# Optimization experiments

Hardware: AMD Instinct MI355X
Metric: run time of the kernel (lower is better)

## Reference

```python
import jax, jax.numpy as jnp
import numpy as np

B, T, H, DH = 4, 2048, 16, 64   # batch, block_size, num_head, chunk_size (per-head dim)
NE = H * DH                      # n_embed = 1024
EPS = 1e-5                       # torch GroupNorm default eps


def _decay_mask(T):
    # D[h, n, m] = gamma_h**(n-m) for n>=m else 0 (RetNet decay matrix)
    gamma = 1.0 - 2.0 ** (-5.0 - jnp.arange(H, dtype=jnp.float32))  # [H]
    idx = jnp.arange(T)
    diff = idx[:, None] - idx[None, :]                # [T, T]
    mask = diff >= 0
    expo = jnp.where(mask, diff, 0).astype(jnp.float32)
    D = (gamma[:, None, None] ** expo[None]) * mask[None].astype(jnp.float32)
    return gamma, D


def setup_inputs() -> dict:
    key = jax.random.key(0)
    ks = jax.random.split(key, 5)
    x = jax.random.normal(ks[0], (B, T, NE), jnp.float32)
    past_kv = jax.random.normal(ks[1], (H, DH, DH), jnp.float32)
    Wq = jax.random.normal(ks[2], (NE, NE), jnp.float32) * 0.02
    Wk = jax.random.normal(ks[3], (NE, NE), jnp.float32) * 0.02
    Wv = jax.random.normal(ks[4], (NE, NE), jnp.float32) * 0.02
    gn_w = jnp.ones((H,), jnp.float32)
    gn_b = jnp.zeros((H,), jnp.float32)
    return {"x": x, "past_kv": past_kv, "Wq": Wq, "Wk": Wk, "Wv": Wv,
            "gn_w": gn_w, "gn_b": gn_b}


def reference(x, past_kv, Wq, Wk, Wv, gn_w, gn_b):
    b, t, c = x.shape
    gamma, D = _decay_mask(t)                                  # [H], [H,T,T]

    def split_heads(y):
        return y.reshape(b, t, H, DH).transpose(0, 2, 1, 3)    # [B,H,T,DH]

    q = split_heads(x @ Wq)
    k = split_heads(x @ Wk)
    v = split_heads(x @ Wv)

    # intra-chunk retention: (Q K^T) * D
    retention = jnp.einsum('bhtd,bhsd->bhts', q, k) * D[None]  # [B,H,T,T]
    inner = jnp.einsum('bhts,bhsd->bhtd', retention, v)        # [B,H,T,DH]

    # cross-chunk term (faithful to source): ((q @ past_kv)^T @ D)^T
    pp = jnp.einsum('bhtd,hde->bhte', q, past_kv)              # [B,H,T,DH]
    cross = jnp.einsum('hst,bhse->bhte', D, pp)                # [B,H,T,DH]

    ret = inner + cross                                        # [B,H,T,DH]

    # GroupNorm(1, H) over channels-first layout [B, H, DH, T]
    y = ret.transpose(0, 1, 3, 2)                              # [B,H,DH,T]
    mu = y.mean(axis=(1, 2, 3), keepdims=True)
    var = y.var(axis=(1, 2, 3), keepdims=True)                 # biased, as torch
    yn = (y - mu) / jnp.sqrt(var + EPS)
    yn = yn * gn_w[None, :, None, None] + gn_b[None, :, None, None]

    # rearrange 'b c h t -> b t (c h)' with (c=H, h=DH)
    out = yn.transpose(0, 3, 1, 2).reshape(b, t, H * DH)       # [B,T,NE]

    # recurrent state update: gamma * past_kv + K^T V, batch-averaged
    current_kv = gamma[:, None, None] * past_kv[None] + \
                 jnp.einsum('bhtd,bhte->bhde', k, v)           # [B,H,DH,DH]
    return out, current_kv.mean(axis=0)
```

## Files before the change

kernel.cpp:

```cpp
#include <hip/hip_runtime.h>
#include <stdint.h>

typedef float v4f __attribute__((ext_vector_type(4)));
typedef short v8s __attribute__((ext_vector_type(8)));

#define SZ_BHTD 8388608
#define SZ_HTD  131072

#define GL2LDS(g, l) __builtin_amdgcn_global_load_lds( \
    (const __attribute__((address_space(1))) void*)(g), \
    (__attribute__((address_space(3))) void*)(l), 16, 0, 0)

__device__ __forceinline__ uint16_t f2bf(float f){
  uint32_t u = __float_as_uint(f);
  u += 0x7fffu + ((u >> 16) & 1u);
  return (uint16_t)(u >> 16);
}
__device__ __forceinline__ float bf2f(uint16_t v){
  return __uint_as_float(((uint32_t)v) << 16);
}

__global__ __launch_bounds__(256) void k_conv(const float* __restrict__ x,
                                              const float* __restrict__ Wq, const float* __restrict__ Wk,
                                              const float* __restrict__ Wv,
                                              uint16_t* __restrict__ xb, uint16_t* __restrict__ wt){
  if (blockIdx.x < 8192){
    int i = blockIdx.x*256 + threadIdx.x;
    const float4 v = ((const float4*)x)[i];
    ushort4 o; o.x = f2bf(v.x); o.y = f2bf(v.y); o.z = f2bf(v.z); o.w = f2bf(v.w);
    ((ushort4*)xb)[i] = o;
    return;
  }
  __shared__ float t[64][65];
  const int blk2 = blockIdx.x - 8192;
  const int z = blk2 >> 8, y = (blk2 >> 4) & 15, xx = blk2 & 15;
  const float* W = z==0 ? Wq : (z==1 ? Wk : Wv);
  int n0 = xx*64, k0 = y*64;
  for (int idx = threadIdx.x; idx < 4096; idx += 256){
    int r = idx >> 6, c = idx & 63;
    t[r][c] = W[(k0+r)*1024 + n0 + c];
  }
  __syncthreads();
  for (int idx = threadIdx.x; idx < 4096; idx += 256){
    int r = idx >> 6, c = idx & 63;
    wt[(size_t)(z*1024 + n0 + r)*1024 + k0 + c] = f2bf(t[c][r]);
  }
}

__global__ __launch_bounds__(256) void k_gemm(const uint16_t* __restrict__ Xb, const uint16_t* __restrict__ Wt,
                                              uint16_t* __restrict__ qkv){
  __shared__ uint16_t As[128*64];
  __shared__ uint16_t Bs[128*64];
  const int tid = threadIdx.x;
  const int lane = tid & 63, w = tid >> 6;
  const int quad = lane >> 4, l16 = lane & 15;
  const int wm = (w >> 1)*64, wn = (w & 1)*64;
  const int bm = blockIdx.x, bn = blockIdx.y;
  v4f acc[4][4] = {};
  const uint16_t* Ag = Xb + (size_t)(bm*128)*1024;
  const uint16_t* Bg = Wt + (size_t)(bn*128)*1024;
  const int rA = lane >> 3;
  const int ce = (((lane & 7) ^ rA) * 8);
  const int xr = l16 & 7;
  for (int k0 = 0; k0 < 1024; k0 += 64){
    #pragma unroll
    for (int j = 0; j < 4; ++j){
      const int cA = w*4 + j;
      const int r = cA*8 + rA;
      GL2LDS(Ag + (size_t)r*1024 + k0 + ce, As + cA*512);
      GL2LDS(Bg + (size_t)r*1024 + k0 + ce, Bs + cA*512);
    }
    __syncthreads();
    #pragma unroll
    for (int kk = 0; kk < 64; kk += 32){
      const int ch = ((quad + (kk >> 3)) ^ xr) * 8;
      v8s a[4], b[4];
      #pragma unroll
      for (int u = 0; u < 4; ++u) a[u] = *(v8s*)&As[(wm + u*16 + l16)*64 + ch];
      #pragma unroll
      for (int u = 0; u < 4; ++u) b[u] = *(v8s*)&Bs[(wn + u*16 + l16)*64 + ch];
      #pragma unroll
      for (int mi = 0; mi < 4; ++mi)
        #pragma unroll
        for (int ni = 0; ni < 4; ++ni)
          acc[mi][ni] = __builtin_amdgcn_mfma_f32_16x16x32_bf16(a[mi], b[ni], acc[mi][ni], 0, 0, 0);
    }
    __syncthreads();
  }
  #pragma unroll
  for (int mi = 0; mi < 4; ++mi){
    #pragma unroll
    for (int ni = 0; ni < 4; ++ni){
      int n = bn*128 + wn + ni*16 + l16;
      int which = n >> 10, cch = n & 1023;
      int hh = cch >> 6, dd = cch & 63;
      #pragma unroll
      for (int r = 0; r < 4; ++r){
        int m = bm*128 + wm + mi*16 + quad*4 + r;
        int b = m >> 11, t = m & 2047;
        qkv[(size_t)which*SZ_BHTD + (size_t)((b*16 + hh)*2048 + t)*64 + dd] = f2bf(acc[mi][ni][r]);
      }
    }
  }
}

__global__ __launch_bounds__(256) void k_pre(const uint16_t* __restrict__ qkv, const float* __restrict__ pkv,
                                             uint16_t* __restrict__ UT, uint16_t* __restrict__ ckp,
                                             float* __restrict__ headv){
  __shared__ uint16_t KTb[64*72];
  __shared__ uint16_t VTb[64*72];
  __shared__ uint16_t VTw[64*72];
  __shared__ float tab[65];
  __shared__ float qbar[64];
  const int tid = threadIdx.x, blk = blockIdx.x;
  const int bh = blk >> 5, c = blk & 31, h = bh & 15;
  const int lane = tid & 63, w = tid >> 6;
  const int quad = lane >> 4, l16 = lane & 15;
  const float g = 1.0f - exp2f(-(float)(5 + h));
  if (tid <= 64) tab[tid] = powf(g, (float)tid);
  const uint16_t* Qg = qkv + (size_t)bh*SZ_HTD + c*4096;
  const uint16_t* Kg = Qg + SZ_BHTD;
  const uint16_t* Vg = Qg + 2*(size_t)SZ_BHTD;
  const float* Pg = pkv + h*4096;
  __syncthreads();
  #pragma unroll
  for (int it = 0; it < 16; ++it){
    int idx = it*256 + tid;
    int s = idx >> 6, d = idx & 63;
    uint16_t kv = Kg[idx], vv = Vg[idx];
    KTb[d*72 + s] = kv;
    VTb[d*72 + s] = vv;
    VTw[d*72 + s] = f2bf(tab[63 - s]*bf2f(vv));
  }
  if (tid < 64){
    float acc = 0.f;
    for (int j = 0; j < 64; ++j) acc = fmaf(tab[j], bf2f(Qg[j*64 + tid]), acc);
    qbar[tid] = acc;
  }
  __syncthreads();
  const int ar = (w*16 + l16)*72 + quad*8;
  v8s aK0 = *(v8s*)&KTb[ar], aK1 = *(v8s*)&KTb[ar + 32];
  v8s aW0 = *(v8s*)&VTw[ar], aW1 = *(v8s*)&VTw[ar + 32];
  v4f accC[4] = {}, accU[4] = {};
  #pragma unroll
  for (int ni = 0; ni < 4; ++ni){
    const int br = (ni*16 + l16)*72 + quad*8;
    v8s bV0 = *(v8s*)&VTb[br], bV1 = *(v8s*)&VTb[br + 32];
    v8s bK0 = *(v8s*)&KTb[br], bK1 = *(v8s*)&KTb[br + 32];
    accC[ni] = __builtin_amdgcn_mfma_f32_16x16x32_bf16(aK0, bV0, accC[ni], 0, 0, 0);
    accC[ni] = __builtin_amdgcn_mfma_f32_16x16x32_bf16(aK1, bV1, accC[ni], 0, 0, 0);
    accU[ni] = __builtin_amdgcn_mfma_f32_16x16x32_bf16(aW0, bK0, accU[ni], 0, 0, 0);
    accU[ni] = __builtin_amdgcn_mfma_f32_16x16x32_bf16(aW1, bK1, accU[ni], 0, 0, 0);
  }
  const size_t ob = (size_t)blk*4096;
  #pragma unroll
  for (int ni = 0; ni < 4; ++ni){
    int e = ni*16 + l16;
    #pragma unroll
    for (int r = 0; r < 4; ++r){
      int d = w*16 + quad*4 + r;
      ckp[ob + d*64 + e] = f2bf(accC[ni][r]);
      UT[ob + d*64 + e]  = f2bf(accU[ni][r]);
    }
  }
  if (tid < 64){
    float acc = 0.f;
    for (int dd = 0; dd < 64; ++dd) acc = fmaf(qbar[dd], Pg[dd*64 + tid], acc);
    headv[(size_t)blk*64 + tid] = acc;
  }
}

__global__ __launch_bounds__(256) void k_scan(const uint16_t* __restrict__ UT, uint16_t* __restrict__ S,
                                              const float* __restrict__ headv, float* __restrict__ tailv){
  if (blockIdx.x < 256){
    const int bh = blockIdx.x >> 2, part = blockIdx.x & 3, h = bh & 15;
    const float g = 1.0f - exp2f(-(float)(5 + h));
    const float g64 = powf(g, 64.0f);
    const int off = part*1024 + threadIdx.x*4;
    float st0=0.f, st1=0.f, st2=0.f, st3=0.f;
    for (int c = 0; c < 32; ++c){
      const size_t base = ((size_t)bh*32 + c)*4096 + off;
      ushort4 u = *(const ushort4*)&UT[base];
      ushort4 o; o.x=f2bf(st0); o.y=f2bf(st1); o.z=f2bf(st2); o.w=f2bf(st3);
      *(ushort4*)&S[base] = o;
      st0 = fmaf(g64, st0, bf2f(u.x)); st1 = fmaf(g64, st1, bf2f(u.y));
      st2 = fmaf(g64, st2, bf2f(u.z)); st3 = fmaf(g64, st3, bf2f(u.w));
    }
    return;
  }
  const int lin = (blockIdx.x - 256)*256 + threadIdx.x;
  const int bh = lin >> 6, e = lin & 63, h = bh & 15;
  const float g = 1.0f - exp2f(-(float)(5 + h));
  const float g64 = powf(g, 64.0f);
  float R = 0.0f;
  for (int c = 31; c >= 0; --c){
    const size_t o = ((size_t)bh*32 + c)*64 + e;
    tailv[o] = R;
    R = fmaf(g64, R, headv[o]);
  }
}

__global__ __launch_bounds__(256) void k_main(const uint16_t* __restrict__ qkv, const uint16_t* __restrict__ Sg_,
                                              const float* __restrict__ pkv, const float* __restrict__ tailv,
                                              uint16_t* __restrict__ ret, float2* __restrict__ pb){
  __shared__ uint16_t Qb[64*72];
  __shared__ uint16_t Kb[64*72];
  __shared__ uint16_t VTb[64*72];
  __shared__ uint16_t B2[64*72];
  __shared__ uint16_t Sb[64*72];
  __shared__ float tab[65];
  __shared__ float ps[8];
  const int tid = threadIdx.x, blk = blockIdx.x;
  const int bh = blk >> 5, c = blk & 31, h = bh & 15;
  const int lane = tid & 63, w = tid >> 6;
  const int quad = lane >> 4, l16 = lane & 15;
  const float g = 1.0f - exp2f(-(float)(5 + h));
  if (tid <= 64) tab[tid] = powf(g, (float)tid);
  const uint16_t* Qg = qkv + (size_t)bh*SZ_HTD + c*4096;
  const uint16_t* Kg = Qg + SZ_BHTD;
  const uint16_t* Vg = Qg + 2*(size_t)SZ_BHTD;
  const uint16_t* Sgp = Sg_ + (size_t)blk*4096;
  const float* Pg = pkv + h*4096;
  #pragma unroll
  for (int v = 0; v < 2; ++v){
    int idx = (tid*2 + v)*8;
    int r = idx >> 6, cc = idx & 63;
    *(uint4*)&Qb[r*72 + cc] = *(const uint4*)&Qg[idx];
    *(uint4*)&Kb[r*72 + cc] = *(const uint4*)&Kg[idx];
    *(uint4*)&Sb[r*72 + cc] = *(const uint4*)&Sgp[idx];
  }
  #pragma unroll
  for (int it = 0; it < 16; ++it){
    int idx = it*256 + tid;
    int r = idx >> 6, cc = idx & 63;
    VTb[cc*72 + r] = Vg[idx];
    B2[cc*72 + r] = f2bf(Pg[idx]);
  }
  __syncthreads();
  const int ar = (w*16 + l16)*72 + quad*8;
  v8s aQ0 = *(v8s*)&Qb[ar], aQ1 = *(v8s*)&Qb[ar + 32];
  v4f accP[4] = {}, accPP[4] = {}, accIT[4] = {};
  #pragma unroll
  for (int ni = 0; ni < 4; ++ni){
    const int br = (ni*16 + l16)*72 + quad*8;
    v8s b0 = *(v8s*)&Kb[br], b1 = *(v8s*)&Kb[br + 32];
    accP[ni] = __builtin_amdgcn_mfma_f32_16x16x32_bf16(aQ0, b0, accP[ni], 0, 0, 0);
    accP[ni] = __builtin_amdgcn_mfma_f32_16x16x32_bf16(aQ1, b1, accP[ni], 0, 0, 0);
    v8s c0 = *(v8s*)&B2[br], c1 = *(v8s*)&B2[br + 32];
    accPP[ni] = __builtin_amdgcn_mfma_f32_16x16x32_bf16(aQ0, c0, accPP[ni], 0, 0, 0);
    accPP[ni] = __builtin_amdgcn_mfma_f32_16x16x32_bf16(aQ1, c1, accPP[ni], 0, 0, 0);
    v8s d0 = *(v8s*)&Sb[br], d1 = *(v8s*)&Sb[br + 32];
    accIT[ni] = __builtin_amdgcn_mfma_f32_16x16x32_bf16(aQ0, d0, accIT[ni], 0, 0, 0);
    accIT[ni] = __builtin_amdgcn_mfma_f32_16x16x32_bf16(aQ1, d1, accIT[ni], 0, 0, 0);
  }
  __syncthreads();
  #pragma unroll
  for (int ni = 0; ni < 4; ++ni){
    #pragma unroll
    for (int r = 0; r < 4; ++r){
      int i = w*16 + quad*4 + r;
      int j = ni*16 + l16;
      Kb[i*72 + j] = f2bf((i >= j) ? accP[ni][r]*tab[i - j] : 0.0f);
      B2[j*72 + i] = f2bf(accPP[ni][r]);
    }
  }
  __syncthreads();
  v8s aP0 = *(v8s*)&Kb[ar], aP1 = *(v8s*)&Kb[ar + 32];
  v8s aM0, aM1;
  {
    int i = w*16 + l16;
    #pragma unroll
    for (int u = 0; u < 8; ++u){
      int j0 = quad*8 + u, j1 = 32 + quad*8 + u;
      aM0[u] = (short)f2bf((j0 >= i) ? tab[j0 - i] : 0.0f);
      aM1[u] = (short)f2bf((j1 >= i) ? tab[j1 - i] : 0.0f);
    }
  }
  v4f accI[4] = {}, accX[4] = {};
  #pragma unroll
  for (int ni = 0; ni < 4; ++ni){
    const int br = (ni*16 + l16)*72 + quad*8;
    v8s b0 = *(v8s*)&VTb[br], b1 = *(v8s*)&VTb[br + 32];
    accI[ni] = __builtin_amdgcn_mfma_f32_16x16x32_bf16(aP0, b0, accI[ni], 0, 0, 0);
    accI[ni] = __builtin_amdgcn_mfma_f32_16x16x32_bf16(aP1, b1, accI[ni], 0, 0, 0);
    v8s e0 = *(v8s*)&B2[br], e1 = *(v8s*)&B2[br + 32];
    accX[ni] = __builtin_amdgcn_mfma_f32_16x16x32_bf16(aM0, e0, accX[ni], 0, 0, 0);
    accX[ni] = __builtin_amdgcn_mfma_f32_16x16x32_bf16(aM1, e1, accX[ni], 0, 0, 0);
  }
  const size_t rbase = (size_t)bh*2048 + (size_t)c*64;
  float s1 = 0.f, s2 = 0.f;
  #pragma unroll
  for (int ni = 0; ni < 4; ++ni){
    int d = ni*16 + l16;
    float tl = tailv[(size_t)blk*64 + d];
    #pragma unroll
    for (int r = 0; r < 4; ++r){
      int i = w*16 + quad*4 + r;
      float v = accI[ni][r] + tab[i + 1]*accIT[ni][r] + accX[ni][r] + tab[64 - i]*tl;
      ret[(rbase + i)*64 + d] = f2bf(v);
      s1 += v; s2 += v*v;
    }
  }
  #pragma unroll
  for (int off = 32; off > 0; off >>= 1){
    s1 += __shfl_down(s1, off);
    s2 += __shfl_down(s2, off);
  }
  if (lane == 0){ ps[w*2] = s1; ps[w*2+1] = s2; }
  __syncthreads();
  if (tid == 0){
    float2 o; o.x = ps[0] + ps[2] + ps[4] + ps[6];
    o.y = ps[1] + ps[3] + ps[5] + ps[7];
    pb[blk] = o;
  }
}

__global__ __launch_bounds__(256) void k_stats(const float2* __restrict__ pb, float* __restrict__ stats){
  __shared__ float ps[8];
  const int b = blockIdx.x;
  float s = 0.0f, s2 = 0.0f;
  for (int i = threadIdx.x; i < 512; i += 256){
    const float2 p = pb[(size_t)b*512 + i];
    s += p.x; s2 += p.y;
  }
  #pragma unroll
  for (int off = 32; off > 0; off >>= 1){
    s  += __shfl_down(s, off);
    s2 += __shfl_down(s2, off);
  }
  const int wv = threadIdx.x >> 6;
  if ((threadIdx.x & 63) == 0){ ps[wv*2] = s; ps[wv*2+1] = s2; }
  __syncthreads();
  if (threadIdx.x == 0){
    stats[b*2]   = ps[0] + ps[2] + ps[4] + ps[6];
    stats[b*2+1] = ps[1] + ps[3] + ps[5] + ps[7];
  }
}

__global__ __launch_bounds__(256) void k_norm(const uint16_t* __restrict__ ret, const float* __restrict__ stats,
                                              const float* __restrict__ gw, const float* __restrict__ gb,
                                              float* __restrict__ out){
  const int o = (blockIdx.x*256 + threadIdx.x)*4;
  const int b = o >> 21, t = (o >> 10) & 2047, cch = o & 1023;
  const int h = cch >> 6, d = cch & 63;
  const float inv = 1.0f/2097152.0f;
  const float mu = stats[b*2]*inv;
  const float var = stats[b*2+1]*inv - mu*mu;
  const float rs = rsqrtf(var + 1e-5f);
  const float w = gw[h]*rs, bb = gb[h];
  const ushort4 v = *(const ushort4*)&ret[((size_t)(b*16 + h)*2048 + t)*64 + d];
  float4 r;
  r.x = (bf2f(v.x) - mu)*w + bb; r.y = (bf2f(v.y) - mu)*w + bb;
  r.z = (bf2f(v.z) - mu)*w + bb; r.w = (bf2f(v.w) - mu)*w + bb;
  *(float4*)&out[o] = r;
}

__global__ __launch_bounds__(64) void k_ckb(const float* __restrict__ pkv, const uint16_t* __restrict__ ckp,
                                            float* __restrict__ out2){
  const int lin = blockIdx.x*64 + threadIdx.x;
  const int i = lin*4;
  const int h = i >> 12, de = i & 4095;
  const float g = 1.0f - exp2f(-(float)(5 + h));
  float acc[4] = {0.0f, 0.0f, 0.0f, 0.0f};
  for (int b = 0; b < 4; ++b){
    const uint16_t* base = ckp + ((size_t)(b*16 + h)*32)*4096 + de;
    for (int c = 0; c < 32; ++c){
      #pragma unroll
      for (int u = 0; u < 4; ++u) acc[u] += bf2f(base[(size_t)c*4096 + u]);
    }
  }
  #pragma unroll
  for (int u = 0; u < 4; ++u)
    out2[i + u] = fmaf(g, pkv[i + u], 0.25f*acc[u]);
}

extern "C" void kernel_launch(void* const* d_in, const int* in_sizes, int n_in,
                              void* d_out, int out_size, void* d_ws, size_t ws_size,
                              hipStream_t stream){
  const float* x   = (const float*)d_in[0];
  const float* pkv = (const float*)d_in[1];
  const float* Wq  = (const float*)d_in[2];
  const float* Wk  = (const float*)d_in[3];
  const float* Wv  = (const float*)d_in[4];
  const float* gnw = (const float*)d_in[5];
  const float* gnb = (const float*)d_in[6];
  float* out  = (float*)d_out;
  float* out2 = out + 8388608;

  char* ws = (char*)d_ws;
  size_t off = 0;
  float*    stats = (float*)(ws + off);    off += 256;
  float2*   pb    = (float2*)(ws + off);   off += (size_t)8192*8;
  uint16_t* Xb    = (uint16_t*)(ws + off); off += (size_t)8388608*2;
  uint16_t* Wt    = (uint16_t*)(ws + off); off += (size_t)3145728*2;
  uint16_t* QKV   = (uint16_t*)(ws + off); off += (size_t)3*8388608*2;
  uint16_t* ret   = (uint16_t*)(ws + off); off += (size_t)8388608*2;
  uint16_t* UT    = (uint16_t*)(ws + off); off += (size_t)8388608*2;
  uint16_t* S     = (uint16_t*)(ws + off); off += (size_t)8388608*2;
  uint16_t* CKp   = (uint16_t*)(ws + off); off += (size_t)8388608*2;
  float*    headv = (float*)(ws + off);    off += (size_t)131072*4;
  float*    tailv = (float*)(ws + off);    off += (size_t)131072*4;

  k_conv<<<8960, 256, 0, stream>>>(x, Wq, Wk, Wv, Xb, Wt);
  k_gemm<<<dim3(64, 24), 256, 0, stream>>>(Xb, Wt, QKV);
  k_pre<<<2048, 256, 0, stream>>>(QKV, pkv, UT, CKp, headv);
  k_scan<<<272, 256, 0, stream>>>(UT, S, headv, tailv);
  k_main<<<2048, 256, 0, stream>>>(QKV, S, pkv, tailv, ret, pb);
  k_stats<<<4, 256, 0, stream>>>(pb, stats);
  k_norm<<<8192, 256, 0, stream>>>(ret, stats, gnw, gnb, out);
  k_ckb<<<256, 64, 0, stream>>>(pkv, CKp, out2);
}
```

Before: 254.2 us.

## Parallelize k_pre reductions across warps, widen scan grid, merge ckb with stats

In k_pre, the qbar and headv dot products now run on all four waves, each handling a quarter of the reduction, with the partial sums combined through shared memory. Before, one wave did this serially while the other three sat idle. The chunk scan now uses one thread per element across 1024 blocks instead of ushort4 vectors across 256 blocks, which gives more parallelism but narrower loads. The k_stats and k_ckb kernels are merged into a single launch, saving one kernel launch at the cost of extra syncs in k_pre.

```diff
diff --git a/kernel.cpp b/kernel.cpp
--- a/kernel.cpp
+++ b/kernel.cpp
@@ -112,6 +112,7 @@
   __shared__ uint16_t VTw[64*72];
   __shared__ float tab[65];
   __shared__ float qbar[64];
+  __shared__ float part4[4][64];
   const int tid = threadIdx.x, blk = blockIdx.x;
   const int bh = blk >> 5, c = blk & 31, h = bh & 15;
   const int lane = tid & 63, w = tid >> 6;
@@ -132,12 +133,17 @@
     VTb[d*72 + s] = vv;
     VTw[d*72 + s] = f2bf(tab[63 - s]*bf2f(vv));
   }
-  if (tid < 64){
+  {
     float acc = 0.f;
-    for (int j = 0; j < 64; ++j) acc = fmaf(tab[j], bf2f(Qg[j*64 + tid]), acc);
-    qbar[tid] = acc;
-  }
-  __syncthreads();
+    #pragma unroll
+    for (int jj = 0; jj < 16; ++jj){
+      int j = w*16 + jj;
+      acc = fmaf(tab[j], bf2f(Qg[j*64 + lane]), acc);
+    }
+    part4[w][lane] = acc;
+  }
+  __syncthreads();
+  if (tid < 64) qbar[tid] = part4[0][tid] + part4[1][tid] + part4[2][tid] + part4[3][tid];
   const int ar = (w*16 + l16)*72 + quad*8;
   v8s aK0 = *(v8s*)&KTb[ar], aK1 = *(v8s*)&KTb[ar + 32];
   v8s aW0 = *(v8s*)&VTw[ar], aW1 = *(v8s*)&VTw[ar + 32];
@@ -163,32 +169,38 @@
       UT[ob + d*64 + e]  = f2bf(accU[ni][r]);
     }
   }
-  if (tid < 64){
+  __syncthreads();
+  {
     float acc = 0.f;
-    for (int dd = 0; dd < 64; ++dd) acc = fmaf(qbar[dd], Pg[dd*64 + tid], acc);
-    headv[(size_t)blk*64 + tid] = acc;
-  }
+    #pragma unroll
+    for (int dd = 0; dd < 16; ++dd){
+      int d = w*16 + dd;
+      acc = fmaf(qbar[d], Pg[d*64 + lane], acc);
+    }
+    part4[w][lane] = acc;
+  }
+  __syncthreads();
+  if (tid < 64)
+    headv[(size_t)blk*64 + tid] = part4[0][tid] + part4[1][tid] + part4[2][tid] + part4[3][tid];
 }
 
 __global__ __launch_bounds__(256) void k_scan(const uint16_t* __restrict__ UT, uint16_t* __restrict__ S,
                                               const float* __restrict__ headv, float* __restrict__ tailv){
-  if (blockIdx.x < 256){
-    const int bh = blockIdx.x >> 2, part = blockIdx.x & 3, h = bh & 15;
+  if (blockIdx.x < 1024){
+    const int lin = blockIdx.x*256 + threadIdx.x;
+    const int bh = lin >> 12, off = lin & 4095, h = bh & 15;
     const float g = 1.0f - exp2f(-(float)(5 + h));
     const float g64 = powf(g, 64.0f);
-    const int off = part*1024 + threadIdx.x*4;
-    float st0=0.f, st1=0.f, st2=0.f, st3=0.f;
+    float st = 0.f;
     for (int c = 0; c < 32; ++c){
-      const size_t base = ((size_t)bh*32 + c)*4096 + off;
-      ushort4 u = *(const ushort4*)&UT[base];
-      ushort4 o; o.x=f2bf(st0); o.y=f2bf(st1); o.z=f2bf(st2); o.w=f2bf(st3);
-      *(ushort4*)&S[base] = o;
-      st0 = fmaf(g64, st0, bf2f(u.x)); st1 = fmaf(g64, st1, bf2f(u.y));
-      st2 = fmaf(g64, st2, bf2f(u.z)); st3 = fmaf(g64, st3, bf2f(u.w));
+      const size_t base = ((size_t)(bh*32 + c))*4096 + off;
+      uint16_t u = UT[base];
+      S[base] = f2bf(st);
+      st = fmaf(g64, st, bf2f(u));
     }
     return;
   }
-  const int lin = (blockIdx.x - 256)*256 + threadIdx.x;
+  const int lin = (blockIdx.x - 1024)*256 + threadIdx.x;
   const int bh = lin >> 6, e = lin & 63, h = bh & 15;
   const float g = 1.0f - exp2f(-(float)(5 + h));
   const float g64 = powf(g, 64.0f);
@@ -315,11 +327,30 @@
   }
 }
 
-__global__ __launch_bounds__(256) void k_stats(const float2* __restrict__ pb, float* __restrict__ stats){
-  __shared__ float ps[8];
-  const int b = blockIdx.x;
+__global__ __launch_bounds__(64) void k_ckbs(const float* __restrict__ pkv, const uint16_t* __restrict__ ckp,
+                                             const float2* __restrict__ pb, float* __restrict__ out2,
+                                             float* __restrict__ stats){
+  if (blockIdx.x < 256){
+    const int lin = blockIdx.x*64 + threadIdx.x;
+    const int i = lin*4;
+    const int h = i >> 12, de = i & 4095;
+    const float g = 1.0f - exp2f(-(float)(5 + h));
+    float acc[4] = {0.0f, 0.0f, 0.0f, 0.0f};
+    for (int b = 0; b < 4; ++b){
+      const uint16_t* base = ckp + ((size_t)(b*16 + h)*32)*4096 + de;
+      for (int c = 0; c < 32; ++c){
+        #pragma unroll
+        for (int u = 0; u < 4; ++u) acc[u] += bf2f(base[(size_t)c*4096 + u]);
+      }
+    }
+    #pragma unroll
+    for (int u = 0; u < 4; ++u)
+      out2[i + u] = fmaf(g, pkv[i + u], 0.25f*acc[u]);
+    return;
+  }
+  const int b = blockIdx.x - 256;
   float s = 0.0f, s2 = 0.0f;
-  for (int i = threadIdx.x; i < 512; i += 256){
+  for (int i = threadIdx.x; i < 512; i += 64){
     const float2 p = pb[(size_t)b*512 + i];
     s += p.x; s2 += p.y;
   }
@@ -328,12 +359,9 @@
     s  += __shfl_down(s, off);
     s2 += __shfl_down(s2, off);
   }
-  const int wv = threadIdx.x >> 6;
-  if ((threadIdx.x & 63) == 0){ ps[wv*2] = s; ps[wv*2+1] = s2; }
-  __syncthreads();
   if (threadIdx.x == 0){
-    stats[b*2]   = ps[0] + ps[2] + ps[4] + ps[6];
-    stats[b*2+1] = ps[1] + ps[3] + ps[5] + ps[7];
+    stats[b*2]   = s;
+    stats[b*2+1] = s2;
   }
 }
 
@@ -355,25 +383,6 @@
   *(float4*)&out[o] = r;
 }
 
-__global__ __launch_bounds__(64) void k_ckb(const float* __restrict__ pkv, const uint16_t* __restrict__ ckp,
-                                            float* __restrict__ out2){
-  const int lin = blockIdx.x*64 + threadIdx.x;
-  const int i = lin*4;
-  const int h = i >> 12, de = i & 4095;
-  const float g = 1.0f - exp2f(-(float)(5 + h));
-  float acc[4] = {0.0f, 0.0f, 0.0f, 0.0f};
-  for (int b = 0; b < 4; ++b){
-    const uint16_t* base = ckp + ((size_t)(b*16 + h)*32)*4096 + de;
-    for (int c = 0; c < 32; ++c){
-      #pragma unroll
-      for (int u = 0; u < 4; ++u) acc[u] += bf2f(base[(size_t)c*4096 + u]);
-    }
-  }
-  #pragma unroll
-  for (int u = 0; u < 4; ++u)
-    out2[i + u] = fmaf(g, pkv[i + u], 0.25f*acc[u]);
-}
-
 extern "C" void kernel_launch(void* const* d_in, const int* in_sizes, int n_in,
                               void* d_out, int out_size, void* d_ws, size_t ws_size,
                               hipStream_t stream){
@@ -404,9 +413,8 @@
   k_conv<<<8960, 256, 0, stream>>>(x, Wq, Wk, Wv, Xb, Wt);
   k_gemm<<<dim3(64, 24), 256, 0, stream>>>(Xb, Wt, QKV);
   k_pre<<<2048, 256, 0, stream>>>(QKV, pkv, UT, CKp, headv);
-  k_scan<<<272, 256, 0, stream>>>(UT, S, headv, tailv);
+  k_scan<<<1040, 256, 0, stream>>>(UT, S, headv, tailv);
   k_main<<<2048, 256, 0, stream>>>(QKV, S, pkv, tailv, ret, pb);
-  k_stats<<<4, 256, 0, stream>>>(pb, stats);
+  k_ckbs<<<260, 64, 0, stream>>>(pkv, CKp, pb, out2, stats);
   k_norm<<<8192, 256, 0, stream>>>(ret, stats, gnw, gnb, out);
-  k_ckb<<<256, 64, 0, stream>>>(pkv, CKp, out2);
-}
+}
```

Result: no change. 254.4 us (+0.1%).
